# Performance work log

Hardware: AMD Instinct MI355X
Metric: run time of the kernel (lower is better)

Reference implementation:

```python
import jax, jax.numpy as jnp
import numpy as np

N, E = 50000, 800000
H, C = 4, 32          # heads, per-head channels
IN_DIM = 128
NEG_SLOPE = 0.2


def gat_conv(x, edge_index, W, a_src, a_dst, b):
    """PyG-style GATConv: Wx, per-edge leaky-relu logits, dst-segment softmax,
    scatter-weighted aggregation, concat heads, add bias. Self-loops added."""
    n = x.shape[0]
    loops = jnp.arange(n, dtype=edge_index.dtype)
    src = jnp.concatenate([edge_index[0], loops])
    dst = jnp.concatenate([edge_index[1], loops])
    xw = (x @ W).reshape(n, H, C)                      # [N,H,C]
    alpha_src = jnp.sum(xw * a_src, axis=-1)           # [N,H]
    alpha_dst = jnp.sum(xw * a_dst, axis=-1)           # [N,H]
    e = jax.nn.leaky_relu(alpha_src[src] + alpha_dst[dst], NEG_SLOPE)  # [E+N,H]
    m = jax.ops.segment_max(e, dst, num_segments=n)    # stable softmax per dst
    e = jnp.exp(e - m[dst])
    denom = jax.ops.segment_sum(e, dst, num_segments=n)
    alpha = e / denom[dst]                             # [E+N,H]
    out = jax.ops.segment_sum(alpha[:, :, None] * xw[src], dst, num_segments=n)
    return out.reshape(n, H * C) + b


def setup_inputs() -> dict:
    key = jax.random.key(0)
    ks = jax.random.split(key, 12)
    HC = H * C
    x = jax.random.normal(ks[0], (N, IN_DIM), dtype=jnp.float32)
    edge_index = jax.random.randint(ks[1], (2, E), 0, N, dtype=jnp.int32)
    s0 = 1.0 / np.sqrt(IN_DIM)
    s1 = 1.0 / np.sqrt(HC)
    return {
        "x": x,
        "edge_index": edge_index,
        "W0": jax.random.normal(ks[2], (IN_DIM, HC), dtype=jnp.float32) * s0,
        "a_src0": jax.random.normal(ks[3], (H, C), dtype=jnp.float32) * s1,
        "a_dst0": jax.random.normal(ks[4], (H, C), dtype=jnp.float32) * s1,
        "b0": jnp.zeros((HC,), dtype=jnp.float32),
        "W1": jax.random.normal(ks[5], (HC, HC), dtype=jnp.float32) * s1,
        "a_src1": jax.random.normal(ks[6], (H, C), dtype=jnp.float32) * s1,
        "a_dst1": jax.random.normal(ks[7], (H, C), dtype=jnp.float32) * s1,
        "b1": jnp.zeros((HC,), dtype=jnp.float32),
        "Wr": jax.random.normal(ks[8], (HC, 1), dtype=jnp.float32) * s1,
        "br": jnp.zeros((1,), dtype=jnp.float32),
    }


def reference(x, edge_index, W0, a_src0, a_dst0, b0, W1, a_src1, a_dst1, b1, Wr, br):
    h = jax.nn.elu(gat_conv(x, edge_index, W0, a_src0, a_dst0, b0))
    # F.dropout(training=False) -> identity (eval mode)
    h = jax.nn.elu(gat_conv(h, edge_index, W1, a_src1, a_dst1, b1))
    return h @ Wr + br
```

## Files before the change

kernel.cpp:

```cpp
#include <hip/hip_runtime.h>
#include <hip/hip_bf16.h>
#include <hip/hip_fp16.h>

#define DEV __device__ __forceinline__

DEV float lrelu(float x) { return x > 0.f ? x : 0.2f * x; }
DEV float elu(float x)   { return x > 0.f ? x : __expf(x) - 1.f; }

#define CAP 64

__global__ __launch_bounds__(256, 5)
void gemm0_scatter(const float* __restrict__ X, const float* __restrict__ W,
                   const float* __restrict__ a_src, const float* __restrict__ a_dst,
                   __half2* __restrict__ xw2, float* __restrict__ asrc,
                   float* __restrict__ adst, int n, int gblk,
                   const int* __restrict__ ei, int* __restrict__ deg,
                   int* __restrict__ col2, int E, int sblk) {
    if ((int)blockIdx.x >= gblk) {
        int stride = sblk * 256;
        for (int e = ((int)blockIdx.x - gblk) * 256 + (int)threadIdx.x; e < E;
             e += stride) {
            int s = ei[e], d = ei[E + e];
            int pos = atomicAdd(&deg[d], 1);
            if (pos < CAP) col2[d * CAP + pos] = s;
        }
        return;
    }
    __shared__ float Xs[32][68];
    __shared__ float Ws[32][132];
    int t = threadIdx.x;
    int n0 = (int)blockIdx.x * 64;
    int rg = t >> 4;
    int cg = t & 15;
    int q0 = cg * 8 + ((cg >= 8) ? 4 : 0);

    float acc[4][8];
#pragma unroll
    for (int r = 0; r < 4; ++r)
#pragma unroll
        for (int c = 0; c < 8; ++c) acc[r][c] = 0.f;

    float4 px[2], pw[4];
    auto load_x = [&](int k0, float4* p) {
#pragma unroll
        for (int it = 0; it < 2; ++it) {
            int idx = t + it * 256;
            int row = idx >> 3, kq = idx & 7;
            int gr = n0 + row;
            p[it] = (gr < n) ? *(const float4*)&X[(size_t)gr * 128 + k0 + kq * 4]
                             : make_float4(0.f, 0.f, 0.f, 0.f);
        }
    };
    auto load_w = [&](int k0, float4* p) {
#pragma unroll
        for (int it = 0; it < 4; ++it) {
            int idx = t + it * 256;
            int k = idx >> 5, cq = idx & 31;
            p[it] = *(const float4*)&W[(size_t)(k0 + k) * 128 + cq * 4];
        }
    };
    auto store_lds = [&](const float4* pX, const float4* pW) {
#pragma unroll
        for (int it = 0; it < 2; ++it) {
            int idx = t + it * 256;
            int row = idx >> 3, kq = idx & 7;
            Xs[kq * 4 + 0][row] = pX[it].x;
            Xs[kq * 4 + 1][row] = pX[it].y;
            Xs[kq * 4 + 2][row] = pX[it].z;
            Xs[kq * 4 + 3][row] = pX[it].w;
        }
#pragma unroll
        for (int it = 0; it < 4; ++it) {
            int idx = t + it * 256;
            int k = idx >> 5, cq = idx & 31;
            *(float4*)&Ws[k][cq * 4 + ((cq >= 16) ? 4 : 0)] = pW[it];
        }
    };

    load_x(0, px);
    load_w(0, pw);
    for (int c4 = 0; c4 < 4; ++c4) {
        store_lds(px, pw);
        __syncthreads();
        if (c4 < 3) { load_x((c4 + 1) * 32, px); load_w((c4 + 1) * 32, pw); }
#pragma unroll 4
        for (int k = 0; k < 32; ++k) {
            float4 xv = *(const float4*)&Xs[k][rg * 4];
            float4 w0 = *(const float4*)&Ws[k][q0];
            float4 w1 = *(const float4*)&Ws[k][q0 + 4];
            float xr[4] = {xv.x, xv.y, xv.z, xv.w};
            float wr[8] = {w0.x, w0.y, w0.z, w0.w, w1.x, w1.y, w1.z, w1.w};
#pragma unroll
            for (int r = 0; r < 4; ++r)
#pragma unroll
                for (int c = 0; c < 8; ++c)
                    acc[r][c] = fmaf(xr[r], wr[c], acc[r][c]);
        }
        __syncthreads();
    }

    int c0 = cg * 8;
    int h = cg >> 2;
    float as8[8], ad8[8];
#pragma unroll
    for (int c = 0; c < 8; ++c) { as8[c] = a_src[c0 + c]; ad8[c] = a_dst[c0 + c]; }
#pragma unroll
    for (int r = 0; r < 4; ++r) {
        int gr = n0 + rg * 4 + r;
        float s_ = 0.f, d_ = 0.f;
#pragma unroll
        for (int c = 0; c < 8; ++c) {
            s_ = fmaf(acc[r][c], as8[c], s_);
            d_ = fmaf(acc[r][c], ad8[c], d_);
        }
        s_ += __shfl_xor(s_, 1); s_ += __shfl_xor(s_, 2);
        d_ += __shfl_xor(d_, 1); d_ += __shfl_xor(d_, 2);
        if (gr < n) {
            __half2* rowp = &xw2[(size_t)gr * 64 + (c0 >> 1)];
            rowp[0] = __floats2half2_rn(acc[r][0], acc[r][1]);
            rowp[1] = __floats2half2_rn(acc[r][2], acc[r][3]);
            rowp[2] = __floats2half2_rn(acc[r][4], acc[r][5]);
            rowp[3] = __floats2half2_rn(acc[r][6], acc[r][7]);
            if ((t & 3) == 0) { asrc[gr * 4 + h] = s_; adst[gr * 4 + h] = d_; }
        }
    }
}

__global__ __launch_bounds__(512, 8)
void agg0_gemm1(const __half2* __restrict__ xw2a, const float* __restrict__ asrc0,
                const float* __restrict__ adst0, const int* __restrict__ col2,
                const int* __restrict__ deg, const float* __restrict__ bias,
                const float* __restrict__ W, const float* __restrict__ a_src,
                const float* __restrict__ a_dst, __half2* __restrict__ xw2b,
                float* __restrict__ asrc1, float* __restrict__ adst1, int n) {
    __shared__ __half Xh[128 * 66];
    __shared__ float Ws[32][132];
    int t = threadIdx.x;
    int n0 = (int)blockIdx.x * 64;
    int l = t & 63;
    int q = t >> 6;

    float4 pw[2];
    auto load_w = [&](int k0, float4* p) {
#pragma unroll
        for (int it = 0; it < 2; ++it) {
            int idx = t + it * 512;
            int k = idx >> 5, cq = idx & 31;
            p[it] = *(const float4*)&W[(size_t)(k0 + k) * 128 + cq * 4];
        }
    };
    auto store_w = [&](const float4* p) {
#pragma unroll
        for (int it = 0; it < 2; ++it) {
            int idx = t + it * 512;
            int k = idx >> 5, cq = idx & 31;
            *(float4*)&Ws[k][cq * 4 + ((cq >= 16) ? 4 : 0)] = p[it];
        }
    };
    load_w(0, pw);

    {
        int h4 = l & 3;
        int jj = l >> 2;
        int hA = l >> 4;
        for (int it = 0; it < 8; ++it) {
            int i = __builtin_amdgcn_readfirstlane(n0 + q * 8 + it);
            float rx = 0.f, ry = 0.f;
            if (i < n) {
                int beg = i * CAP;
                int dcount = deg[i]; if (dcount > CAP) dcount = CAP;
                int end = beg + dcount;
                float ad = adst0[i * 4 + h4];
                float wsum = __expf(lrelu(asrc0[i * 4 + h4] + ad));
                float wselfA = __shfl(wsum, hA);
                float2 row_i = __half22float2(xw2a[(size_t)i * 64 + l]);
                float2 a0 = make_float2(wselfA * row_i.x, wselfA * row_i.y);
                float2 a1 = make_float2(0.f, 0.f);
                float2 a2 = make_float2(0.f, 0.f);
                float2 a3 = make_float2(0.f, 0.f);
                int ce = beg;
                for (; ce + 16 <= end; ce += 16) {
                    int s = col2[ce + jj];
                    float wv = __expf(lrelu(asrc0[s * 4 + h4] + ad));
                    float sv = wv;
                    sv += __shfl_xor(sv, 4);
                    sv += __shfl_xor(sv, 8);
                    sv += __shfl_xor(sv, 16);
                    sv += __shfl_xor(sv, 32);
                    wsum += sv;
#pragma unroll
                    for (int j = 0; j < 16; j += 4) {
                        int s0 = col2[ce + j + 0];
                        int s1 = col2[ce + j + 1];
                        int s2 = col2[ce + j + 2];
                        int s3 = col2[ce + j + 3];
                        float g0 = __shfl(wv, (j + 0) * 4 + hA);
                        float g1 = __shfl(wv, (j + 1) * 4 + hA);
                        float g2 = __shfl(wv, (j + 2) * 4 + hA);
                        float g3 = __shfl(wv, (j + 3) * 4 + hA);
                        float2 v0 = __half22float2(xw2a[(size_t)s0 * 64 + l]);
                        float2 v1 = __half22float2(xw2a[(size_t)s1 * 64 + l]);
                        float2 v2 = __half22float2(xw2a[(size_t)s2 * 64 + l]);
                        float2 v3 = __half22float2(xw2a[(size_t)s3 * 64 + l]);
                        a0.x = fmaf(g0, v0.x, a0.x); a0.y = fmaf(g0, v0.y, a0.y);
                        a1.x = fmaf(g1, v1.x, a1.x); a1.y = fmaf(g1, v1.y, a1.y);
                        a2.x = fmaf(g2, v2.x, a2.x); a2.y = fmaf(g2, v2.y, a2.y);
                        a3.x = fmaf(g3, v3.x, a3.x); a3.y = fmaf(g3, v3.y, a3.y);
                    }
                }
                if (ce < end) {
                    int nc = end - ce;
                    float wv = 0.f;
                    if (jj < nc) {
                        int s = col2[ce + jj];
                        wv = __expf(lrelu(asrc0[s * 4 + h4] + ad));
                    }
                    float sv = wv;
                    sv += __shfl_xor(sv, 4);
                    sv += __shfl_xor(sv, 8);
                    sv += __shfl_xor(sv, 16);
                    sv += __shfl_xor(sv, 32);
                    wsum += sv;
#pragma unroll
                    for (int j = 0; j < 16; ++j) {
                        if (j >= nc) break;
                        int sj = col2[ce + j];
                        float wg = __shfl(wv, j * 4 + hA);
                        float2 v = __half22float2(xw2a[(size_t)sj * 64 + l]);
                        a0.x = fmaf(wg, v.x, a0.x);
                        a0.y = fmaf(wg, v.y, a0.y);
                    }
                }
                a0.x += (a1.x + a2.x) + a3.x;
                a0.y += (a1.y + a2.y) + a3.y;
                float wsA = __shfl(wsum, hA);
                float inv = 1.f / wsA;
                float2 bv = *(const float2*)&bias[2 * l];
                rx = elu(a0.x * inv + bv.x);
                ry = elu(a0.y * inv + bv.y);
            }
            int row = q * 8 + it;
            Xh[(2 * l) * 66 + row]     = __float2half(rx);
            Xh[(2 * l + 1) * 66 + row] = __float2half(ry);
        }
    }
    __syncthreads();

    int rg = t >> 4;
    int cg = t & 15;
    int q0 = cg * 8 + ((cg >= 8) ? 4 : 0);
    float acc[2][8];
#pragma unroll
    for (int r = 0; r < 2; ++r)
#pragma unroll
        for (int c = 0; c < 8; ++c) acc[r][c] = 0.f;

    for (int c4 = 0; c4 < 4; ++c4) {
        store_w(pw);
        __syncthreads();
        if (c4 < 3) load_w((c4 + 1) * 32, pw);
        int kb = c4 * 32;
#pragma unroll 4
        for (int k = 0; k < 32; ++k) {
            float2 xv = __half22float2(*(const __half2*)&Xh[(kb + k) * 66 + rg * 2]);
            float4 w0 = *(const float4*)&Ws[k][q0];
            float4 w1 = *(const float4*)&Ws[k][q0 + 4];
            float wr[8] = {w0.x, w0.y, w0.z, w0.w, w1.x, w1.y, w1.z, w1.w};
#pragma unroll
            for (int c = 0; c < 8; ++c) {
                acc[0][c] = fmaf(xv.x, wr[c], acc[0][c]);
                acc[1][c] = fmaf(xv.y, wr[c], acc[1][c]);
            }
        }
        __syncthreads();
    }

    int c0 = cg * 8;
    int h = cg >> 2;
    float as8[8], ad8[8];
#pragma unroll
    for (int c = 0; c < 8; ++c) { as8[c] = a_src[c0 + c]; ad8[c] = a_dst[c0 + c]; }
#pragma unroll
    for (int r = 0; r < 2; ++r) {
        int gr = n0 + rg * 2 + r;
        float s_ = 0.f, d_ = 0.f;
#pragma unroll
        for (int c = 0; c < 8; ++c) {
            s_ = fmaf(acc[r][c], as8[c], s_);
            d_ = fmaf(acc[r][c], ad8[c], d_);
        }
        s_ += __shfl_xor(s_, 1); s_ += __shfl_xor(s_, 2);
        d_ += __shfl_xor(d_, 1); d_ += __shfl_xor(d_, 2);
        if (gr < n) {
            __half2* rowp = &xw2b[(size_t)gr * 64 + (c0 >> 1)];
            rowp[0] = __floats2half2_rn(acc[r][0], acc[r][1]);
            rowp[1] = __floats2half2_rn(acc[r][2], acc[r][3]);
            rowp[2] = __floats2half2_rn(acc[r][4], acc[r][5]);
            rowp[3] = __floats2half2_rn(acc[r][6], acc[r][7]);
            if ((t & 3) == 0) { asrc1[gr * 4 + h] = s_; adst1[gr * 4 + h] = d_; }
        }
    }
}

__global__ __launch_bounds__(256, 8)
void aggregate_v7(const __half2* __restrict__ xw2, const float* __restrict__ asrc,
                  const float* __restrict__ adst, const int* __restrict__ col2,
                  const int* __restrict__ deg, const float* __restrict__ bias,
                  float* __restrict__ out1, const float* __restrict__ Wr,
                  const float* __restrict__ br, int n) {
    int l = threadIdx.x & 63;
    int i = __builtin_amdgcn_readfirstlane((blockIdx.x * 256 + threadIdx.x) >> 6);
    if (i >= n) return;
    int h4 = l & 3;
    int jj = l >> 2;
    int hA = l >> 4;
    int beg = i * CAP;
    int dcount = deg[i]; if (dcount > CAP) dcount = CAP;
    int end = beg + dcount;
    float ad = adst[i * 4 + h4];
    float wsum = __expf(lrelu(asrc[i * 4 + h4] + ad));
    float wselfA = __shfl(wsum, hA);
    float2 row_i = __half22float2(xw2[(size_t)i * 64 + l]);
    float2 a0 = make_float2(wselfA * row_i.x, wselfA * row_i.y);
    float2 a1 = make_float2(0.f, 0.f);
    float2 a2 = make_float2(0.f, 0.f);
    float2 a3 = make_float2(0.f, 0.f);

    int ce = beg;
    for (; ce + 16 <= end; ce += 16) {
        int s = col2[ce + jj];
        float wv = __expf(lrelu(asrc[s * 4 + h4] + ad));
        float sv = wv;
        sv += __shfl_xor(sv, 4);
        sv += __shfl_xor(sv, 8);
        sv += __shfl_xor(sv, 16);
        sv += __shfl_xor(sv, 32);
        wsum += sv;
#pragma unroll
        for (int j = 0; j < 16; j += 4) {
            int s0 = col2[ce + j + 0];
            int s1 = col2[ce + j + 1];
            int s2 = col2[ce + j + 2];
            int s3 = col2[ce + j + 3];
            float g0 = __shfl(wv, (j + 0) * 4 + hA);
            float g1 = __shfl(wv, (j + 1) * 4 + hA);
            float g2 = __shfl(wv, (j + 2) * 4 + hA);
            float g3 = __shfl(wv, (j + 3) * 4 + hA);
            float2 v0 = __half22float2(xw2[(size_t)s0 * 64 + l]);
            float2 v1 = __half22float2(xw2[(size_t)s1 * 64 + l]);
            float2 v2 = __half22float2(xw2[(size_t)s2 * 64 + l]);
            float2 v3 = __half22float2(xw2[(size_t)s3 * 64 + l]);
            a0.x = fmaf(g0, v0.x, a0.x); a0.y = fmaf(g0, v0.y, a0.y);
            a1.x = fmaf(g1, v1.x, a1.x); a1.y = fmaf(g1, v1.y, a1.y);
            a2.x = fmaf(g2, v2.x, a2.x); a2.y = fmaf(g2, v2.y, a2.y);
            a3.x = fmaf(g3, v3.x, a3.x); a3.y = fmaf(g3, v3.y, a3.y);
        }
    }
    if (ce < end) {
        int nc = end - ce;
        float wv = 0.f;
        if (jj < nc) {
            int s = col2[ce + jj];
            wv = __expf(lrelu(asrc[s * 4 + h4] + ad));
        }
        float sv = wv;
        sv += __shfl_xor(sv, 4);
        sv += __shfl_xor(sv, 8);
        sv += __shfl_xor(sv, 16);
        sv += __shfl_xor(sv, 32);
        wsum += sv;
#pragma unroll
        for (int j = 0; j < 16; ++j) {
            if (j >= nc) break;
            int sj = col2[ce + j];
            float wg = __shfl(wv, j * 4 + hA);
            float2 v = __half22float2(xw2[(size_t)sj * 64 + l]);
            a0.x = fmaf(wg, v.x, a0.x);
            a0.y = fmaf(wg, v.y, a0.y);
        }
    }
    a0.x += (a1.x + a2.x) + a3.x;
    a0.y += (a1.y + a2.y) + a3.y;
    float wsA = __shfl(wsum, hA);
    float inv = 1.f / wsA;
    float2 bv = *(const float2*)&bias[2 * l];
    float rx = elu(a0.x * inv + bv.x);
    float ry = elu(a0.y * inv + bv.y);
    float v = rx * Wr[2 * l] + ry * Wr[2 * l + 1];
#pragma unroll
    for (int off = 32; off > 0; off >>= 1) v += __shfl_xor(v, off);
    if (l == 0) out1[i] = v + br[0];
}

extern "C" void kernel_launch(void* const* d_in, const int* in_sizes, int n_in,
                              void* d_out, int out_size, void* d_ws, size_t ws_size,
                              hipStream_t stream) {
    const float* x   = (const float*)d_in[0];
    const int*   ei  = (const int*)d_in[1];
    const float* W0  = (const float*)d_in[2];
    const float* as0 = (const float*)d_in[3];
    const float* ad0 = (const float*)d_in[4];
    const float* b0  = (const float*)d_in[5];
    const float* W1  = (const float*)d_in[6];
    const float* as1 = (const float*)d_in[7];
    const float* ad1 = (const float*)d_in[8];
    const float* b1  = (const float*)d_in[9];
    const float* Wr  = (const float*)d_in[10];
    const float* br  = (const float*)d_in[11];
    float* out = (float*)d_out;

    const int N = in_sizes[0] / 128;
    const int E = in_sizes[1] / 2;

    char* w = (char*)d_ws;
    size_t off = 0;
    auto alloc = [&](size_t bytes) -> void* {
        void* p = w + off;
        off += (bytes + 255) & ~size_t(255);
        return p;
    };
    __half2* xw2a  = (__half2*)alloc((size_t)N * 64 * 4);
    __half2* xw2b  = (__half2*)alloc((size_t)N * 64 * 4);
    float* asrc0   = (float*)alloc((size_t)N * 4 * 4);
    float* adst0   = (float*)alloc((size_t)N * 4 * 4);
    float* asrc1   = (float*)alloc((size_t)N * 4 * 4);
    float* adst1   = (float*)alloc((size_t)N * 4 * 4);
    int*   deg     = (int*)alloc((size_t)N * 4);
    int*   col2    = (int*)alloc((size_t)N * CAP * 4);

    hipMemsetAsync(deg, 0, (size_t)N * 4, stream);

    const int gblk = (N + 63) / 64;
    const int sblk = 768;
    const int ablk = (N + 3) / 4;
    gemm0_scatter<<<gblk + sblk, 256, 0, stream>>>(x, W0, as0, ad0, xw2a, asrc0,
                                                   adst0, N, gblk, ei, deg, col2,
                                                   E, sblk);
    agg0_gemm1<<<gblk, 512, 0, stream>>>(xw2a, asrc0, adst0, col2, deg, b0,
                                         W1, as1, ad1, xw2b, asrc1, adst1, N);
    aggregate_v7<<<ablk, 256, 0, stream>>>(xw2b, asrc1, adst1, col2, deg, b1,
                                           out, Wr, br, N);
}
```

Measured before the change: 282.5 us.

## Use fp16 packed dot2 for both dense GEMMs with half2 LDS tiles

Both the layer-0 GEMM and the fused layer-1 GEMM now store X and W tiles in LDS as K-paired half2 values and accumulate with v_dot2_f32_f16, which halves LDS footprint and the FMA instruction count. The gemm0 kernel's occupancy hint is raised from 5 to 8 blocks per CU to exploit the smaller shared-memory usage. Inputs are rounded to fp16 before multiplication, which lowers precision of the projections and the attention logits and may affect tolerance.

```diff
diff --git a/kernel.cpp b/kernel.cpp
--- a/kernel.cpp
+++ b/kernel.cpp
@@ -7,9 +7,16 @@
 DEV float lrelu(float x) { return x > 0.f ? x : 0.2f * x; }
 DEV float elu(float x)   { return x > 0.f ? x : __expf(x) - 1.f; }
 
+typedef _Float16 v2h __attribute__((ext_vector_type(2)));
+DEV float fdot2(__half2 a, __half2 b, float c) {
+    union { __half2 h; v2h v; } ua, ub;
+    ua.h = a; ub.h = b;
+    return __builtin_amdgcn_fdot2(ua.v, ub.v, c, false);
+}
+
 #define CAP 64
 
-__global__ __launch_bounds__(256, 5)
+__global__ __launch_bounds__(256, 8)
 void gemm0_scatter(const float* __restrict__ X, const float* __restrict__ W,
                    const float* __restrict__ a_src, const float* __restrict__ a_dst,
                    __half2* __restrict__ xw2, float* __restrict__ asrc,
@@ -26,8 +33,8 @@
         }
         return;
     }
-    __shared__ float Xs[32][68];
-    __shared__ float Ws[32][132];
+    __shared__ __half2 Xs2[16][68];
+    __shared__ __half2 Ws2[16][132];
     int t = threadIdx.x;
     int n0 = (int)blockIdx.x * 64;
     int rg = t >> 4;
@@ -53,10 +60,11 @@
     };
     auto load_w = [&](int k0, float4* p) {
 #pragma unroll
-        for (int it = 0; it < 4; ++it) {
+        for (int it = 0; it < 2; ++it) {
             int idx = t + it * 256;
-            int k = idx >> 5, cq = idx & 31;
-            p[it] = *(const float4*)&W[(size_t)(k0 + k) * 128 + cq * 4];
+            int k2 = idx >> 5, cq = idx & 31;
+            p[2 * it]     = *(const float4*)&W[(size_t)(k0 + 2 * k2) * 128 + cq * 4];
+            p[2 * it + 1] = *(const float4*)&W[(size_t)(k0 + 2 * k2 + 1) * 128 + cq * 4];
         }
     };
     auto store_lds = [&](const float4* pX, const float4* pW) {
@@ -64,16 +72,20 @@
         for (int it = 0; it < 2; ++it) {
             int idx = t + it * 256;
             int row = idx >> 3, kq = idx & 7;
-            Xs[kq * 4 + 0][row] = pX[it].x;
-            Xs[kq * 4 + 1][row] = pX[it].y;
-            Xs[kq * 4 + 2][row] = pX[it].z;
-            Xs[kq * 4 + 3][row] = pX[it].w;
-        }
-#pragma unroll
-        for (int it = 0; it < 4; ++it) {
+            Xs2[kq * 2 + 0][row] = __floats2half2_rn(pX[it].x, pX[it].y);
+            Xs2[kq * 2 + 1][row] = __floats2half2_rn(pX[it].z, pX[it].w);
+        }
+#pragma unroll
+        for (int it = 0; it < 2; ++it) {
             int idx = t + it * 256;
-            int k = idx >> 5, cq = idx & 31;
-            *(float4*)&Ws[k][cq * 4 + ((cq >= 16) ? 4 : 0)] = pW[it];
+            int k2 = idx >> 5, cq = idx & 31;
+            const float4 w0 = pW[2 * it], w1 = pW[2 * it + 1];
+            union { __half2 h[4]; float4 f; } u;
+            u.h[0] = __floats2half2_rn(w0.x, w1.x);
+            u.h[1] = __floats2half2_rn(w0.y, w1.y);
+            u.h[2] = __floats2half2_rn(w0.z, w1.z);
+            u.h[3] = __floats2half2_rn(w0.w, w1.w);
+            *(float4*)&Ws2[k2][cq * 4 + ((cq >= 16) ? 4 : 0)] = u.f;
         }
     };
 
@@ -84,17 +96,18 @@
         __syncthreads();
         if (c4 < 3) { load_x((c4 + 1) * 32, px); load_w((c4 + 1) * 32, pw); }
 #pragma unroll 4
-        for (int k = 0; k < 32; ++k) {
-            float4 xv = *(const float4*)&Xs[k][rg * 4];
-            float4 w0 = *(const float4*)&Ws[k][q0];
-            float4 w1 = *(const float4*)&Ws[k][q0 + 4];
-            float xr[4] = {xv.x, xv.y, xv.z, xv.w};
-            float wr[8] = {w0.x, w0.y, w0.z, w0.w, w1.x, w1.y, w1.z, w1.w};
+        for (int k2 = 0; k2 < 16; ++k2) {
+            union { float4 f; __half2 h[4]; } ux, uw0, uw1;
+            ux.f  = *(const float4*)&Xs2[k2][rg * 4];
+            uw0.f = *(const float4*)&Ws2[k2][q0];
+            uw1.f = *(const float4*)&Ws2[k2][q0 + 4];
+            __half2 wr[8] = {uw0.h[0], uw0.h[1], uw0.h[2], uw0.h[3],
+                             uw1.h[0], uw1.h[1], uw1.h[2], uw1.h[3]};
 #pragma unroll
             for (int r = 0; r < 4; ++r)
 #pragma unroll
                 for (int c = 0; c < 8; ++c)
-                    acc[r][c] = fmaf(xr[r], wr[c], acc[r][c]);
+                    acc[r][c] = fdot2(ux.h[r], wr[c], acc[r][c]);
         }
         __syncthreads();
     }
@@ -133,31 +146,29 @@
                 const float* __restrict__ W, const float* __restrict__ a_src,
                 const float* __restrict__ a_dst, __half2* __restrict__ xw2b,
                 float* __restrict__ asrc1, float* __restrict__ adst1, int n) {
-    __shared__ __half Xh[128 * 66];
-    __shared__ float Ws[32][132];
+    __shared__ __half2 Xh2[64][66];
+    __shared__ __half2 Ws2[16][132];
     int t = threadIdx.x;
     int n0 = (int)blockIdx.x * 64;
     int l = t & 63;
     int q = t >> 6;
 
     float4 pw[2];
-    auto load_w = [&](int k0, float4* p) {
-#pragma unroll
-        for (int it = 0; it < 2; ++it) {
-            int idx = t + it * 512;
-            int k = idx >> 5, cq = idx & 31;
-            p[it] = *(const float4*)&W[(size_t)(k0 + k) * 128 + cq * 4];
-        }
-    };
-    auto store_w = [&](const float4* p) {
-#pragma unroll
-        for (int it = 0; it < 2; ++it) {
-            int idx = t + it * 512;
-            int k = idx >> 5, cq = idx & 31;
-            *(float4*)&Ws[k][cq * 4 + ((cq >= 16) ? 4 : 0)] = p[it];
-        }
-    };
-    load_w(0, pw);
+    auto load_w = [&](int k0) {
+        int k2 = t >> 5, cq = t & 31;
+        pw[0] = *(const float4*)&W[(size_t)(k0 + 2 * k2) * 128 + cq * 4];
+        pw[1] = *(const float4*)&W[(size_t)(k0 + 2 * k2 + 1) * 128 + cq * 4];
+    };
+    auto store_w = [&]() {
+        int k2 = t >> 5, cq = t & 31;
+        union { __half2 h[4]; float4 f; } u;
+        u.h[0] = __floats2half2_rn(pw[0].x, pw[1].x);
+        u.h[1] = __floats2half2_rn(pw[0].y, pw[1].y);
+        u.h[2] = __floats2half2_rn(pw[0].z, pw[1].z);
+        u.h[3] = __floats2half2_rn(pw[0].w, pw[1].w);
+        *(float4*)&Ws2[k2][cq * 4 + ((cq >= 16) ? 4 : 0)] = u.f;
+    };
+    load_w(0);
 
     {
         int h4 = l & 3;
@@ -240,8 +251,7 @@
                 ry = elu(a0.y * inv + bv.y);
             }
             int row = q * 8 + it;
-            Xh[(2 * l) * 66 + row]     = __float2half(rx);
-            Xh[(2 * l + 1) * 66 + row] = __float2half(ry);
+            Xh2[l][row] = __floats2half2_rn(rx, ry);
         }
     }
     __syncthreads();
@@ -256,20 +266,23 @@
         for (int c = 0; c < 8; ++c) acc[r][c] = 0.f;
 
     for (int c4 = 0; c4 < 4; ++c4) {
-        store_w(pw);
+        store_w();
         __syncthreads();
-        if (c4 < 3) load_w((c4 + 1) * 32, pw);
-        int kb = c4 * 32;
+        if (c4 < 3) load_w((c4 + 1) * 32);
+        int kb2 = c4 * 16;
 #pragma unroll 4
-        for (int k = 0; k < 32; ++k) {
-            float2 xv = __half22float2(*(const __half2*)&Xh[(kb + k) * 66 + rg * 2]);
-            float4 w0 = *(const float4*)&Ws[k][q0];
-            float4 w1 = *(const float4*)&Ws[k][q0 + 4];
-            float wr[8] = {w0.x, w0.y, w0.z, w0.w, w1.x, w1.y, w1.z, w1.w};
+        for (int k = 0; k < 16; ++k) {
+            __half2 xv0 = Xh2[kb2 + k][rg * 2];
+            __half2 xv1 = Xh2[kb2 + k][rg * 2 + 1];
+            union { float4 f; __half2 h[4]; } uw0, uw1;
+            uw0.f = *(const float4*)&Ws2[k][q0];
+            uw1.f = *(const float4*)&Ws2[k][q0 + 4];
+            __half2 wr[8] = {uw0.h[0], uw0.h[1], uw0.h[2], uw0.h[3],
+                             uw1.h[0], uw1.h[1], uw1.h[2], uw1.h[3]};
 #pragma unroll
             for (int c = 0; c < 8; ++c) {
-                acc[0][c] = fmaf(xv.x, wr[c], acc[0][c]);
-                acc[1][c] = fmaf(xv.y, wr[c], acc[1][c]);
+                acc[0][c] = fdot2(xv0, wr[c], acc[0][c]);
+                acc[1][c] = fdot2(xv1, wr[c], acc[1][c]);
             }
         }
         __syncthreads();
```

After: 281.2 us. Within noise of the previous version (-0.5%).
